# Kernel tuning notes

Hardware: AMD Instinct MI355X
Metric: run time of the kernel (lower is better)

## Reference

```python
import jax, jax.numpy as jnp
import numpy as np

B, SQ, SK, D, N, H = 2, 2048, 2048, 1024, 16, 64
EPS = 1e-5


def setup_inputs() -> dict:
    key = jax.random.key(0)
    ks = jax.random.split(key, 8)
    inv_d = 1.0 / np.sqrt(D)
    inv_h = 1.0 / np.sqrt(H)
    # causal mask: True = masked (filled with -inf), matching torch.where(mask, IGNORE, attn)
    mask = jnp.triu(jnp.ones((SQ, SK), dtype=bool), k=1)
    return {
        "x_q": jax.random.normal(ks[0], (B, SQ, D), dtype=jnp.float32),
        "x_kv": jax.random.normal(ks[1], (B, SK, D), dtype=jnp.float32),
        "mask": mask,
        "W_Q": jax.random.normal(ks[2], (N, D, H), dtype=jnp.float32) * inv_d,
        "W_K": jax.random.normal(ks[3], (N, D, H), dtype=jnp.float32) * inv_d,
        "W_V": jax.random.normal(ks[4], (N, D, H), dtype=jnp.float32) * inv_d,
        "W_O": jax.random.normal(ks[5], (N, H, D), dtype=jnp.float32) * inv_h,
        "b_Q": jnp.zeros((N, H), dtype=jnp.float32),
        "b_K": jnp.zeros((N, H), dtype=jnp.float32),
        "b_V": jnp.zeros((N, H), dtype=jnp.float32),
        "b_O": jnp.zeros((D,), dtype=jnp.float32),
        "ln1_g": jnp.ones((H,), dtype=jnp.float32),
        "ln1_b": jnp.zeros((H,), dtype=jnp.float32),
        "ln2_g": jnp.ones((H,), dtype=jnp.float32),
        "ln2_b": jnp.zeros((H,), dtype=jnp.float32),
    }


def _layernorm(x, g, b):
    # LayerNorm over last dim (d_head), eps=1e-5, biased variance (torch default)
    m = jnp.mean(x, axis=-1, keepdims=True)
    v = jnp.mean(jnp.square(x - m), axis=-1, keepdims=True)
    return (x - m) * jax.lax.rsqrt(v + EPS) * g + b


def reference(x_q, x_kv, mask, W_Q, W_K, W_V, W_O, b_Q, b_K, b_V, b_O,
              ln1_g, ln1_b, ln2_g, ln2_b):
    q = jnp.einsum('bsd,ndh->bsnh', x_q, W_Q) + b_Q    # [B,SQ,N,H]
    k = jnp.einsum('bsd,ndh->bsnh', x_kv, W_K) + b_K   # [B,SK,N,H]
    v = jnp.einsum('bsd,ndh->bsnh', x_kv, W_V) + b_V   # [B,SK,N,H]
    q = _layernorm(q, ln1_g, ln1_b)
    k = _layernorm(k, ln2_g, ln2_b)
    # NOTE: no 1/sqrt(d_head) scaling, faithful to the source module
    attn = jnp.einsum('bqnh,bknh->bnqk', q, k)         # [B,N,SQ,SK]
    attn = jnp.where(mask, -jnp.inf, attn)
    probas = jax.nn.softmax(attn, axis=-1)
    z = jnp.einsum('bnqk,bknh->bqnh', probas, v)       # [B,SQ,N,H]
    out = jnp.einsum('bqnh,nhd->bqd', z, W_O) + b_O    # [B,SQ,D]
    return (out, k, v)
```

## Files before the change

### kernel.cpp

```cpp
#include <hip/hip_runtime.h>
#include <math.h>

namespace {
constexpr int kB  = 2;
constexpr int kS  = 2048;
constexpr int kD  = 1024;
constexpr int kN  = 16;
constexpr int kH  = 64;
constexpr int kBS = kB * kS;
constexpr int kNH = kN * kH;
}

typedef __bf16 bf16x4 __attribute__((ext_vector_type(4)));
typedef __bf16 bf16x8 __attribute__((ext_vector_type(8)));
typedef float  f32x4  __attribute__((ext_vector_type(4)));

__global__ __launch_bounds__(256) void split_x2(
    const float* __restrict__ in0, const float* __restrict__ in1,
    __bf16* __restrict__ oH0, __bf16* __restrict__ oL0,
    __bf16* __restrict__ oH1, __bf16* __restrict__ oL1)
{
  const int bx = blockIdx.x;
  const float* in;
  __bf16 *oH, *oL;
  long long i4;
  if (bx < 4096) { in = in0; oH = oH0; oL = oL0; i4 = (long long)bx * 256 + threadIdx.x; }
  else           { in = in1; oH = oH1; oL = oL1; i4 = (long long)(bx - 4096) * 256 + threadIdx.x; }
  const float4 v = *(const float4*)(in + i4 * 4);
  const float x[4] = {v.x, v.y, v.z, v.w};
  bf16x4 hi, lo;
#pragma unroll
  for (int i = 0; i < 4; ++i) {
    const __bf16 h = (__bf16)x[i];
    hi[i] = h;
    lo[i] = (__bf16)(x[i] - (float)h);
  }
  *(bf16x4*)(oH + i4 * 4) = hi;
  *(bf16x4*)(oL + i4 * 4) = lo;
}

__global__ __launch_bounds__(256) void transpose_split(
    const float* __restrict__ in, long long hsIn, int ldin,
    __bf16* __restrict__ oH, __bf16* __restrict__ oL, long long hsOut)
{
  __shared__ float T[64][65];
  const int t = threadIdx.x;
  const long long inBase = (long long)blockIdx.z * hsIn +
                           (long long)(blockIdx.x * 64) * ldin + blockIdx.y * 64;
  const long long outBase = (long long)blockIdx.z * hsOut +
                            (long long)(blockIdx.y * 64) * 1024 + blockIdx.x * 64;
#pragma unroll
  for (int rr = 0; rr < 4; ++rr) {
    const int i = rr * 16 + (t >> 4);
    const int j = (t & 15) * 4;
    const float4 v = *(const float4*)(in + inBase + (long long)i * ldin + j);
    T[i][j + 0] = v.x; T[i][j + 1] = v.y; T[i][j + 2] = v.z; T[i][j + 3] = v.w;
  }
  __syncthreads();
#pragma unroll
  for (int rr = 0; rr < 4; ++rr) {
    const int hh = rr * 16 + (t >> 4);
    const int kk = (t & 15) * 4;
    bf16x4 hi, lo;
#pragma unroll
    for (int m = 0; m < 4; ++m) {
      const float x = T[kk + m][hh];
      const __bf16 h = (__bf16)x;
      hi[m] = h;
      lo[m] = (__bf16)(x - (float)h);
    }
    *(bf16x4*)(oH + outBase + (long long)hh * 1024 + kk) = hi;
    *(bf16x4*)(oL + outBase + (long long)hh * 1024 + kk) = lo;
  }
}

__global__ __launch_bounds__(256) void transpose_split_qkv(
    const float* __restrict__ WQ, const float* __restrict__ WK,
    const float* __restrict__ WV,
    __bf16* __restrict__ QH, __bf16* __restrict__ QL,
    __bf16* __restrict__ KHo, __bf16* __restrict__ KLo,
    __bf16* __restrict__ VH, __bf16* __restrict__ VL)
{
  __shared__ float T[64][65];
  const int t = threadIdx.x;
  const int which = blockIdx.z >> 4;
  const int z = blockIdx.z & 15;
  const float* __restrict__ in = (which == 0) ? WQ : (which == 1) ? WK : WV;
  __bf16* __restrict__ oH = (which == 0) ? QH : (which == 1) ? KHo : VH;
  __bf16* __restrict__ oL = (which == 0) ? QL : (which == 1) ? KLo : VL;
  const long long inBase = (long long)z * 65536 +
                           (long long)(blockIdx.x * 64) * 64 + blockIdx.y * 64;
  const long long outBase = (long long)z * 65536 +
                            (long long)(blockIdx.y * 64) * 1024 + blockIdx.x * 64;
#pragma unroll
  for (int rr = 0; rr < 4; ++rr) {
    const int i = rr * 16 + (t >> 4);
    const int j = (t & 15) * 4;
    const float4 v = *(const float4*)(in + inBase + (long long)i * 64 + j);
    T[i][j + 0] = v.x; T[i][j + 1] = v.y; T[i][j + 2] = v.z; T[i][j + 3] = v.w;
  }
  __syncthreads();
#pragma unroll
  for (int rr = 0; rr < 4; ++rr) {
    const int hh = rr * 16 + (t >> 4);
    const int kk = (t & 15) * 4;
    bf16x4 hi, lo;
#pragma unroll
    for (int m = 0; m < 4; ++m) {
      const float x = T[kk + m][hh];
      const __bf16 h = (__bf16)x;
      hi[m] = h;
      lo[m] = (__bf16)(x - (float)h);
    }
    *(bf16x4*)(oH + outBase + (long long)hh * 1024 + kk) = hi;
    *(bf16x4*)(oL + outBase + (long long)hh * 1024 + kk) = lo;
  }
}

__global__ __launch_bounds__(256) void qkv_gemm128p(
    const __bf16* __restrict__ xqH, const __bf16* __restrict__ xqL,
    const __bf16* __restrict__ xkH, const __bf16* __restrict__ xkL,
    const __bf16* __restrict__ WQH, const __bf16* __restrict__ WQL,
    const __bf16* __restrict__ WKH, const __bf16* __restrict__ WKL,
    const __bf16* __restrict__ WVH,
    const float* __restrict__ b_Q, const float* __restrict__ b_K,
    const float* __restrict__ b_V,
    const float* __restrict__ ln1g, const float* __restrict__ ln1b,
    const float* __restrict__ ln2g, const float* __restrict__ ln2b,
    float* __restrict__ out_k, float* __restrict__ out_v,
    __bf16* __restrict__ qH, __bf16* __restrict__ qL,
    __bf16* __restrict__ kHp, __bf16* __restrict__ kLp,
    __bf16* __restrict__ vT)
{
  const int mode = blockIdx.z;
  const int row0 = blockIdx.x * 128;
  const int ct   = blockIdx.y;
  const bool split = (mode < 2);

  __shared__ __align__(16) __bf16 SMEM[20480];
  __bf16 (*ASH)[40] = (__bf16(*)[40])(SMEM);
  __bf16 (*ASL)[40] = (__bf16(*)[40])(SMEM + 5120);
  __bf16 (*BSH)[40] = (__bf16(*)[40])(SMEM + 10240);
  __bf16 (*BSL)[40] = (__bf16(*)[40])(SMEM + 15360);

  const int t = threadIdx.x;
  const int lane = t & 63;
  const int w = t >> 6;
  const int l16 = lane & 15;
  const int quad = lane >> 4;
  const int mBase = (w & 1) * 64;
  const int nBase = (w >> 1) * 64;

  const __bf16* __restrict__ aHp = (mode == 0) ? xqH : xkH;
  const __bf16* __restrict__ aLp = (mode == 0) ? xqL : xkL;
  const __bf16* __restrict__ bHp = (mode == 0) ? WQH : (mode == 1) ? WKH : WVH;
  const __bf16* __restrict__ bLp = (mode == 0) ? WQL : WKL;

  f32x4 acc[4][4] = {};

  const int srow = t >> 1;
  const int skh  = (t & 1) * 16;

  bf16x8 r[8];
  auto loadT = [&](int k0, bf16x8 rr[8]) {
    const long long ga = (long long)(row0 + srow) * 1024 + k0 + skh;
    const long long gb = (long long)(ct * 128 + srow) * 1024 + k0 + skh;
    rr[0] = *(const bf16x8*)(aHp + ga);
    rr[1] = *(const bf16x8*)(aHp + ga + 8);
    rr[2] = *(const bf16x8*)(bHp + gb);
    rr[3] = *(const bf16x8*)(bHp + gb + 8);
    if (split) {
      rr[4] = *(const bf16x8*)(aLp + ga);
      rr[5] = *(const bf16x8*)(aLp + ga + 8);
      rr[6] = *(const bf16x8*)(bLp + gb);
      rr[7] = *(const bf16x8*)(bLp + gb + 8);
    }
  };
  loadT(0, r);

  for (int k0 = 0; k0 < 1024; k0 += 32) {
    if (k0) __syncthreads();
    bf16x8 rn[8];
    if (k0 + 32 < 1024) loadT(k0 + 32, rn);
    *(bf16x8*)&ASH[srow][skh]     = r[0];
    *(bf16x8*)&ASH[srow][skh + 8] = r[1];
    *(bf16x8*)&BSH[srow][skh]     = r[2];
    *(bf16x8*)&BSH[srow][skh + 8] = r[3];
    if (split) {
      *(bf16x8*)&ASL[srow][skh]     = r[4];
      *(bf16x8*)&ASL[srow][skh + 8] = r[5];
      *(bf16x8*)&BSL[srow][skh]     = r[6];
      *(bf16x8*)&BSL[srow][skh + 8] = r[7];
    }
    __syncthreads();

    bf16x8 ah[4], bh[4];
#pragma unroll
    for (int mt = 0; mt < 4; ++mt)
      ah[mt] = *(const bf16x8*)&ASH[mBase + mt * 16 + l16][quad * 8];
#pragma unroll
    for (int nt = 0; nt < 4; ++nt)
      bh[nt] = *(const bf16x8*)&BSH[nBase + nt * 16 + l16][quad * 8];
#pragma unroll
    for (int mt = 0; mt < 4; ++mt)
#pragma unroll
      for (int nt = 0; nt < 4; ++nt)
        acc[mt][nt] = __builtin_amdgcn_mfma_f32_16x16x32_bf16(ah[mt], bh[nt], acc[mt][nt], 0, 0, 0);
    if (split) {
      bf16x8 bl[4];
#pragma unroll
      for (int nt = 0; nt < 4; ++nt)
        bl[nt] = *(const bf16x8*)&BSL[nBase + nt * 16 + l16][quad * 8];
#pragma unroll
      for (int mt = 0; mt < 4; ++mt)
#pragma unroll
        for (int nt = 0; nt < 4; ++nt)
          acc[mt][nt] = __builtin_amdgcn_mfma_f32_16x16x32_bf16(ah[mt], bl[nt], acc[mt][nt], 0, 0, 0);
      bf16x8 al[4];
#pragma unroll
      for (int mt = 0; mt < 4; ++mt)
        al[mt] = *(const bf16x8*)&ASL[mBase + mt * 16 + l16][quad * 8];
#pragma unroll
      for (int mt = 0; mt < 4; ++mt)
#pragma unroll
        for (int nt = 0; nt < 4; ++nt)
          acc[mt][nt] = __builtin_amdgcn_mfma_f32_16x16x32_bf16(al[mt], bh[nt], acc[mt][nt], 0, 0, 0);
    }
#pragma unroll
    for (int i = 0; i < 8; ++i) r[i] = rn[i];
  }

  const float* __restrict__ bias = (mode == 0) ? b_Q : (mode == 1) ? b_K : b_V;
  float bi[4];
#pragma unroll
  for (int nt = 0; nt < 4; ++nt) bi[nt] = bias[ct * 128 + nBase + nt * 16 + l16];

  if (mode <= 1) {
    const float* __restrict__ lg = (mode == 0) ? ln1g : ln2g;
    const float* __restrict__ lb = (mode == 0) ? ln1b : ln2b;
    float gg[4], bb[4];
#pragma unroll
    for (int nt = 0; nt < 4; ++nt) {
      gg[nt] = lg[nt * 16 + l16];
      bb[nt] = lb[nt * 16 + l16];
    }
#pragma unroll
    for (int mt = 0; mt < 4; ++mt)
#pragma unroll
      for (int r4 = 0; r4 < 4; ++r4) {
        float y[4];
#pragma unroll
        for (int nt = 0; nt < 4; ++nt) y[nt] = acc[mt][nt][r4] + bi[nt];
        float s = y[0] + y[1] + y[2] + y[3];
#pragma unroll
        for (int o = 8; o >= 1; o >>= 1) s += __shfl_xor(s, o);
        const float m = s * (1.0f / 64.0f);
        float vs = 0.0f;
#pragma unroll
        for (int nt = 0; nt < 4; ++nt) {
          const float d = y[nt] - m;
          vs += d * d;
        }
#pragma unroll
        for (int o = 8; o >= 1; o >>= 1) vs += __shfl_xor(vs, o);
        const float inv = rsqrtf(vs * (1.0f / 64.0f) + 1e-5f);
#pragma unroll
        for (int nt = 0; nt < 4; ++nt)
          acc[mt][nt][r4] = (y[nt] - m) * inv * gg[nt] + bb[nt];
      }
  } else {
#pragma unroll
    for (int mt = 0; mt < 4; ++mt)
#pragma unroll
      for (int nt = 0; nt < 4; ++nt)
#pragma unroll
        for (int r4 = 0; r4 < 4; ++r4) acc[mt][nt][r4] += bi[nt];
  }

#pragma unroll
  for (int mt = 0; mt < 4; ++mt)
#pragma unroll
    for (int r4 = 0; r4 < 4; ++r4) {
      const long long row = row0 + mBase + mt * 16 + quad * 4 + r4;
      const long long cb = row * 1024 + ct * 128 + nBase;
      if (mode == 0) {
#pragma unroll
        for (int nt = 0; nt < 4; ++nt) {
          const float x = acc[mt][nt][r4];
          const __bf16 h = (__bf16)x;
          qH[cb + nt * 16 + l16] = h;
          qL[cb + nt * 16 + l16] = (__bf16)(x - (float)h);
        }
      } else if (mode == 1) {
#pragma unroll
        for (int nt = 0; nt < 4; ++nt) {
          const float x = acc[mt][nt][r4];
          out_k[cb + nt * 16 + l16] = x;
          const __bf16 h = (__bf16)x;
          kHp[cb + nt * 16 + l16] = h;
          kLp[cb + nt * 16 + l16] = (__bf16)(x - (float)h);
        }
      } else {
#pragma unroll
        for (int nt = 0; nt < 4; ++nt)
          out_v[cb + nt * 16 + l16] = acc[mt][nt][r4];
      }
    }

  if (mode == 2) {
    __syncthreads();
    __bf16* TT = SMEM + w * 4608;
#pragma unroll
    for (int mt = 0; mt < 4; ++mt)
#pragma unroll
      for (int nt = 0; nt < 4; ++nt)
#pragma unroll
        for (int r4 = 0; r4 < 4; ++r4)
          TT[(nt * 16 + l16) * 72 + mt * 16 + quad * 4 + r4] = (__bf16)acc[mt][nt][r4];
    __syncthreads();
    const int b = row0 >> 11;
    const int s0 = (row0 + mBase) & 2047;
    const int head = ct * 2 + (w >> 1);
#pragma unroll
    for (int rep = 0; rep < 8; ++rep) {
      const int h = rep * 8 + (lane >> 3);
      const int s8 = (lane & 7) * 8;
      const bf16x8 vv = *(const bf16x8*)&TT[h * 72 + s8];
      *(bf16x8*)(vT + ((long long)((b * 16 + head) * 64 + h)) * 2048 + s0 + s8) = vv;
    }
  }
}

__global__ __launch_bounds__(256) void ogemm64p(
    const __bf16* __restrict__ zH, const __bf16* __restrict__ WOt,
    const float* __restrict__ b_O, float* __restrict__ out)
{
  const int row0 = blockIdx.x * 64;
  const int ct = blockIdx.y;
  __shared__ __align__(16) __bf16 AS2[2][64][40];
  __shared__ __align__(16) __bf16 BS2[2][128][40];
  const int t = threadIdx.x;
  const int lane = t & 63;
  const int w = t >> 6;
  const int l16 = lane & 15;
  const int quad = lane >> 4;
  const int nBase = w * 32;

  f32x4 acc[4][2] = {};
  const int arow = t >> 2, akh = (t & 3) * 8;
  const int brow = t >> 1, bkh = (t & 1) * 16;

  bf16x8 r0, r1, r2;
  auto loadT = [&](int k0) {
    r0 = *(const bf16x8*)(zH + (long long)(row0 + arow) * 1024 + k0 + akh);
    const long long gb = (long long)(ct * 128 + brow) * 1024 + k0 + bkh;
    r1 = *(const bf16x8*)(WOt + gb);
    r2 = *(const bf16x8*)(WOt + gb + 8);
  };
  loadT(0);
  *(bf16x8*)&AS2[0][arow][akh]     = r0;
  *(bf16x8*)&BS2[0][brow][bkh]     = r1;
  *(bf16x8*)&BS2[0][brow][bkh + 8] = r2;
  __syncthreads();

  for (int k0 = 0; k0 < 1024; k0 += 32) {
    const int cb = (k0 >> 5) & 1;
    const bool more = (k0 + 32 < 1024);
    if (more) loadT(k0 + 32);

    bf16x8 ah[4], bh[2];
#pragma unroll
    for (int mt = 0; mt < 4; ++mt)
      ah[mt] = *(const bf16x8*)&AS2[cb][mt * 16 + l16][quad * 8];
#pragma unroll
    for (int nt = 0; nt < 2; ++nt)
      bh[nt] = *(const bf16x8*)&BS2[cb][nBase + nt * 16 + l16][quad * 8];
#pragma unroll
    for (int mt = 0; mt < 4; ++mt)
#pragma unroll
      for (int nt = 0; nt < 2; ++nt)
        acc[mt][nt] = __builtin_amdgcn_mfma_f32_16x16x32_bf16(ah[mt], bh[nt], acc[mt][nt], 0, 0, 0);

    if (more) {
      const int nb = 1 - cb;
      *(bf16x8*)&AS2[nb][arow][akh]     = r0;
      *(bf16x8*)&BS2[nb][brow][bkh]     = r1;
      *(bf16x8*)&BS2[nb][brow][bkh + 8] = r2;
    }
    __syncthreads();
  }

#pragma unroll
  for (int mt = 0; mt < 4; ++mt)
#pragma unroll
    for (int r4 = 0; r4 < 4; ++r4) {
      const long long row = row0 + mt * 16 + quad * 4 + r4;
#pragma unroll
      for (int nt = 0; nt < 2; ++nt) {
        const int col = ct * 128 + nBase + nt * 16 + l16;
        out[row * 1024 + col] = acc[mt][nt][r4] + b_O[col];
      }
    }
}

__global__ __launch_bounds__(256) void attn_mfma3(
    const __bf16* __restrict__ qHg, const __bf16* __restrict__ qLg,
    const __bf16* __restrict__ kHg, const __bf16* __restrict__ kLg,
    const __bf16* __restrict__ vTg,
    __bf16* __restrict__ zH)
{
  const int p = blockIdx.x;
  const int n = blockIdx.y;
  const int b = blockIdx.z;

  __shared__ __align__(16) __bf16 KH[2][64][72];
  __shared__ __align__(16) __bf16 KL[2][64][72];
  __shared__ __align__(16) __bf16 VS[2][64][72];
  __shared__ __align__(16) __bf16 PS[64][72];

  const int t = threadIdx.x;
  const int lane = t & 63;
  const int w = t >> 6;
  const int l16 = lane & 15;
  const int quad = lane >> 4;
  const int skey = t >> 2;
  const int sh16 = (t & 3) * 16;

  for (int half = 0; half < 2; ++half) {
    const int qt = half ? p : (31 - p);
    const int q0 = qt * 64;

    bf16x8 Qh[2], Ql[2];
    {
      const long long qrow = (long long)(b * kS + q0 + w * 16 + l16) * 1024 + n * 64 + quad * 8;
      Qh[0] = *(const bf16x8*)(qHg + qrow);
      Qh[1] = *(const bf16x8*)(qHg + qrow + 32);
      Ql[0] = *(const bf16x8*)(qLg + qrow);
      Ql[1] = *(const bf16x8*)(qLg + qrow + 32);
    }

    f32x4 O[4] = {};
    float mrow[4] = {-3.0e38f, -3.0e38f, -3.0e38f, -3.0e38f};
    float lrow[4] = {};

    bf16x8 rk0, rk1, rl0, rl1, rv0, rv1;
    auto loadKV = [&](int k0) {
      const long long gk = (long long)(b * kS + k0 + skey) * 1024 + n * 64 + sh16;
      rk0 = *(const bf16x8*)(kHg + gk);
      rk1 = *(const bf16x8*)(kHg + gk + 8);
      rl0 = *(const bf16x8*)(kLg + gk);
      rl1 = *(const bf16x8*)(kLg + gk + 8);
      const long long gv = ((long long)(b * kN + n) * 64 + skey) * 2048 + k0 + sh16;
      rv0 = *(const bf16x8*)(vTg + gv);
      rv1 = *(const bf16x8*)(vTg + gv + 8);
    };
    auto storeKV = [&](int buf) {
      *(bf16x8*)&KH[buf][skey][sh16]     = rk0;
      *(bf16x8*)&KH[buf][skey][sh16 + 8] = rk1;
      *(bf16x8*)&KL[buf][skey][sh16]     = rl0;
      *(bf16x8*)&KL[buf][skey][sh16 + 8] = rl1;
      *(bf16x8*)&VS[buf][skey][sh16]     = rv0;
      *(bf16x8*)&VS[buf][skey][sh16 + 8] = rv1;
    };

    loadKV(0);
    storeKV(0);
    __syncthreads();

    for (int kt = 0; kt <= qt; ++kt) {
      const int cb = kt & 1;
      const bool more = (kt < qt);
      if (more) loadKV((kt + 1) * 64);

      f32x4 S[4] = {};
#pragma unroll
      for (int kc = 0; kc < 4; ++kc) {
        const int row = kc * 16 + l16;
        const bf16x8 kh0 = *(const bf16x8*)&KH[cb][row][quad * 8];
        const bf16x8 kh1 = *(const bf16x8*)&KH[cb][row][32 + quad * 8];
        const bf16x8 kl0 = *(const bf16x8*)&KL[cb][row][quad * 8];
        const bf16x8 kl1 = *(const bf16x8*)&KL[cb][row][32 + quad * 8];
        S[kc] = __builtin_amdgcn_mfma_f32_16x16x32_bf16(Qh[0], kh0, S[kc], 0, 0, 0);
        S[kc] = __builtin_amdgcn_mfma_f32_16x16x32_bf16(Qh[1], kh1, S[kc], 0, 0, 0);
        S[kc] = __builtin_amdgcn_mfma_f32_16x16x32_bf16(Qh[0], kl0, S[kc], 0, 0, 0);
        S[kc] = __builtin_amdgcn_mfma_f32_16x16x32_bf16(Qh[1], kl1, S[kc], 0, 0, 0);
        S[kc] = __builtin_amdgcn_mfma_f32_16x16x32_bf16(Ql[0], kh0, S[kc], 0, 0, 0);
        S[kc] = __builtin_amdgcn_mfma_f32_16x16x32_bf16(Ql[1], kh1, S[kc], 0, 0, 0);
      }

      if (kt == qt) {
        const int k0 = kt * 64;
#pragma unroll
        for (int kc = 0; kc < 4; ++kc) {
          const int key = k0 + kc * 16 + l16;
#pragma unroll
          for (int r4 = 0; r4 < 4; ++r4) {
            const int q = q0 + w * 16 + quad * 4 + r4;
            if (key > q) S[kc][r4] = -3.0e38f;
          }
        }
      }

#pragma unroll
      for (int r4 = 0; r4 < 4; ++r4) {
        float mt = fmaxf(fmaxf(S[0][r4], S[1][r4]), fmaxf(S[2][r4], S[3][r4]));
#pragma unroll
        for (int o = 8; o >= 1; o >>= 1) mt = fmaxf(mt, __shfl_xor(mt, o));
        const float mnew = fmaxf(mrow[r4], mt);
        const float alpha = __expf(mrow[r4] - mnew);
        mrow[r4] = mnew;
        float ls = 0.0f;
#pragma unroll
        for (int kc = 0; kc < 4; ++kc) {
          const float pe = __expf(S[kc][r4] - mnew);
          S[kc][r4] = pe;
          ls += pe;
        }
#pragma unroll
        for (int o = 8; o >= 1; o >>= 1) ls += __shfl_xor(ls, o);
        lrow[r4] = lrow[r4] * alpha + ls;
#pragma unroll
        for (int hc = 0; hc < 4; ++hc) O[hc][r4] *= alpha;
      }

#pragma unroll
      for (int kc = 0; kc < 4; ++kc)
#pragma unroll
        for (int r4 = 0; r4 < 4; ++r4)
          PS[w * 16 + quad * 4 + r4][kc * 16 + l16] = (__bf16)S[kc][r4];

      bf16x8 Pa[2];
#pragma unroll
      for (int c = 0; c < 2; ++c)
        Pa[c] = *(const bf16x8*)&PS[w * 16 + l16][c * 32 + quad * 8];
#pragma unroll
      for (int hc = 0; hc < 4; ++hc) {
        const int hrow = hc * 16 + l16;
        const bf16x8 vb0 = *(const bf16x8*)&VS[cb][hrow][quad * 8];
        const bf16x8 vb1 = *(const bf16x8*)&VS[cb][hrow][32 + quad * 8];
        O[hc] = __builtin_amdgcn_mfma_f32_16x16x32_bf16(Pa[0], vb0, O[hc], 0, 0, 0);
        O[hc] = __builtin_amdgcn_mfma_f32_16x16x32_bf16(Pa[1], vb1, O[hc], 0, 0, 0);
      }

      if (more) storeKV(1 - cb);
      __syncthreads();
    }

#pragma unroll
    for (int r4 = 0; r4 < 4; ++r4) {
      const float inv = 1.0f / lrow[r4];
      const long long zrow = (long long)(b * kS + q0 + w * 16 + quad * 4 + r4) * 1024 + n * 64;
#pragma unroll
      for (int hc = 0; hc < 4; ++hc)
        zH[zrow + hc * 16 + l16] = (__bf16)(O[hc][r4] * inv);
    }
  }
}

__global__ __launch_bounds__(256) void sgemm64(
    const float* __restrict__ A, int lda,
    const float* __restrict__ Bbase, long long bStride, int colMul, int ldb,
    float* __restrict__ C, int ldc,
    const float* __restrict__ bias, int K)
{
  const int row0 = blockIdx.x * 64;
  const int ct = blockIdx.y;
  const float* __restrict__ Bp = Bbase + (long long)ct * bStride;
  const int col0B = ct * colMul;
  const int col0C = ct * 64;
  __shared__ float As[16][68];
  __shared__ float Bs[16][68];
  const int t = threadIdx.x;
  const int ty = t >> 4;
  const int tx = t & 15;
  float acc[4][4] = {};
  for (int k0 = 0; k0 < K; k0 += 16) {
    {
      const int r = t >> 2;
      const int kk = (t & 3) * 4;
      const float4 a4 = *(const float4*)(A + (long long)(row0 + r) * lda + k0 + kk);
      As[kk + 0][r] = a4.x; As[kk + 1][r] = a4.y; As[kk + 2][r] = a4.z; As[kk + 3][r] = a4.w;
    }
    {
      const int kk = t >> 4;
      const int c = (t & 15) * 4;
      *(float4*)&Bs[kk][c] = *(const float4*)(Bp + (long long)(k0 + kk) * ldb + col0B + c);
    }
    __syncthreads();
#pragma unroll
    for (int kk = 0; kk < 16; ++kk) {
      const float4 a4 = *(const float4*)&As[kk][ty * 4];
      const float4 b4 = *(const float4*)&Bs[kk][tx * 4];
      const float av[4] = {a4.x, a4.y, a4.z, a4.w};
      const float bv[4] = {b4.x, b4.y, b4.z, b4.w};
#pragma unroll
      for (int i = 0; i < 4; ++i)
#pragma unroll
        for (int j = 0; j < 4; ++j)
          acc[i][j] = fmaf(av[i], bv[j], acc[i][j]);
    }
    __syncthreads();
  }
#pragma unroll
  for (int i = 0; i < 4; ++i) {
    const int r = row0 + ty * 4 + i;
    float4 o;
    o.x = acc[i][0] + bias[col0C + tx * 4 + 0];
    o.y = acc[i][1] + bias[col0C + tx * 4 + 1];
    o.z = acc[i][2] + bias[col0C + tx * 4 + 2];
    o.w = acc[i][3] + bias[col0C + tx * 4 + 3];
    *(float4*)(C + (long long)r * ldc + col0C + tx * 4) = o;
  }
}

__global__ __launch_bounds__(256) void ln64(
    float* __restrict__ X, const float* __restrict__ g,
    const float* __restrict__ bta, int nrows)
{
  const int row = blockIdx.x * 4 + (threadIdx.x >> 6);
  const int lane = threadIdx.x & 63;
  if (row >= nrows) return;
  const float x = X[(long long)row * 64 + lane];
  float s = x;
#pragma unroll
  for (int o = 32; o >= 1; o >>= 1) s += __shfl_xor(s, o);
  const float m = s * (1.0f / 64.0f);
  const float d = x - m;
  float vs = d * d;
#pragma unroll
  for (int o = 32; o >= 1; o >>= 1) vs += __shfl_xor(vs, o);
  const float inv = rsqrtf(vs * (1.0f / 64.0f) + 1e-5f);
  X[(long long)row * 64 + lane] = d * inv * g[lane] + bta[lane];
}

__global__ __launch_bounds__(256) void attn_mfma(
    const float* __restrict__ Q, const float* __restrict__ Kg,
    const float* __restrict__ Vg, float* __restrict__ Z)
{
  const int qt = (gridDim.x - 1) - blockIdx.x;
  const int n = blockIdx.y;
  const int b = blockIdx.z;
  const int q0 = qt * 64;
  __shared__ __bf16 KH[64][72];
  __shared__ __bf16 KL[64][72];
  __shared__ __bf16 VS[64][72];
  const int t = threadIdx.x;
  const int lane = t & 63;
  const int w = t >> 6;
  const int l16 = lane & 15;
  const int quad = lane >> 4;
  bf16x8 Qh[2], Ql[2];
  {
    const long long qrow = ((long long)(b * kS + q0 + w * 16 + l16)) * kNH + n * kH + quad * 8;
#pragma unroll
    for (int c = 0; c < 2; ++c) {
      const float4 a = *(const float4*)(Q + qrow + c * 32);
      const float4 bq = *(const float4*)(Q + qrow + c * 32 + 4);
      const float x[8] = {a.x, a.y, a.z, a.w, bq.x, bq.y, bq.z, bq.w};
#pragma unroll
      for (int i = 0; i < 8; ++i) {
        const __bf16 h = (__bf16)x[i];
        Qh[c][i] = h;
        Ql[c][i] = (__bf16)(x[i] - (float)h);
      }
    }
  }
  f32x4 O[4] = {};
  float mrow[4] = {-3.0e38f, -3.0e38f, -3.0e38f, -3.0e38f};
  float lrow[4] = {};
  for (int kt = 0; kt <= qt; ++kt) {
    const int k0 = kt * 64;
    __syncthreads();
#pragma unroll
    for (int rep = 0; rep < 4; ++rep) {
      {
        const int row = rep * 16 + (t >> 4);
        const int h4 = (t & 15) * 4;
        const float4 k4 = *(const float4*)(Kg + ((long long)(b * kS + k0 + row)) * kNH + n * kH + h4);
        const float x[4] = {k4.x, k4.y, k4.z, k4.w};
        bf16x4 hi, lo;
#pragma unroll
        for (int i = 0; i < 4; ++i) {
          const __bf16 h = (__bf16)x[i];
          hi[i] = h;
          lo[i] = (__bf16)(x[i] - (float)h);
        }
        *(bf16x4*)&KH[row][h4] = hi;
        *(bf16x4*)&KL[row][h4] = lo;
      }
      {
        const int key = rep * 16 + (t & 15);
        const int h4 = (t >> 4) * 4;
        const float4 v4 = *(const float4*)(Vg + ((long long)(b * kS + k0 + key)) * kNH + n * kH + h4);
        VS[h4 + 0][key] = (__bf16)v4.x;
        VS[h4 + 1][key] = (__bf16)v4.y;
        VS[h4 + 2][key] = (__bf16)v4.z;
        VS[h4 + 3][key] = (__bf16)v4.w;
      }
    }
    __syncthreads();
    f32x4 S[4] = {};
#pragma unroll
    for (int kc = 0; kc < 4; ++kc) {
      const int row = kc * 16 + l16;
      const bf16x8 kh0 = *(const bf16x8*)&KH[row][quad * 8];
      const bf16x8 kh1 = *(const bf16x8*)&KH[row][32 + quad * 8];
      const bf16x8 kl0 = *(const bf16x8*)&KL[row][quad * 8];
      const bf16x8 kl1 = *(const bf16x8*)&KL[row][32 + quad * 8];
      S[kc] = __builtin_amdgcn_mfma_f32_16x16x32_bf16(Qh[0], kh0, S[kc], 0, 0, 0);
      S[kc] = __builtin_amdgcn_mfma_f32_16x16x32_bf16(Qh[1], kh1, S[kc], 0, 0, 0);
      S[kc] = __builtin_amdgcn_mfma_f32_16x16x32_bf16(Qh[0], kl0, S[kc], 0, 0, 0);
      S[kc] = __builtin_amdgcn_mfma_f32_16x16x32_bf16(Qh[1], kl1, S[kc], 0, 0, 0);
      S[kc] = __builtin_amdgcn_mfma_f32_16x16x32_bf16(Ql[0], kh0, S[kc], 0, 0, 0);
      S[kc] = __builtin_amdgcn_mfma_f32_16x16x32_bf16(Ql[1], kh1, S[kc], 0, 0, 0);
    }
    if (kt == qt) {
#pragma unroll
      for (int kc = 0; kc < 4; ++kc) {
        const int key = k0 + kc * 16 + l16;
#pragma unroll
        for (int r = 0; r < 4; ++r) {
          const int q = q0 + w * 16 + quad * 4 + r;
          if (key > q) S[kc][r] = -3.0e38f;
        }
      }
    }
#pragma unroll
    for (int r = 0; r < 4; ++r) {
      float mt = fmaxf(fmaxf(S[0][r], S[1][r]), fmaxf(S[2][r], S[3][r]));
#pragma unroll
      for (int o = 8; o >= 1; o >>= 1) mt = fmaxf(mt, __shfl_xor(mt, o));
      const float mnew = fmaxf(mrow[r], mt);
      const float alpha = __expf(mrow[r] - mnew);
      mrow[r] = mnew;
      float ls = 0.0f;
#pragma unroll
      for (int kc = 0; kc < 4; ++kc) {
        const float pe = __expf(S[kc][r] - mnew);
        S[kc][r] = pe;
        ls += pe;
      }
#pragma unroll
      for (int o = 8; o >= 1; o >>= 1) ls += __shfl_xor(ls, o);
      lrow[r] = lrow[r] * alpha + ls;
#pragma unroll
      for (int hc = 0; hc < 4; ++hc) O[hc][r] *= alpha;
    }
    __syncthreads();
    __bf16(*Ps)[72] = KL;
#pragma unroll
    for (int kc = 0; kc < 4; ++kc)
#pragma unroll
      for (int r = 0; r < 4; ++r)
        Ps[w * 16 + quad * 4 + r][kc * 16 + l16] = (__bf16)S[kc][r];
    bf16x8 Pa[2];
#pragma unroll
    for (int c = 0; c < 2; ++c)
      Pa[c] = *(const bf16x8*)&Ps[w * 16 + l16][c * 32 + quad * 8];
#pragma unroll
    for (int hc = 0; hc < 4; ++hc) {
      const int hrow = hc * 16 + l16;
      const bf16x8 vb0 = *(const bf16x8*)&VS[hrow][quad * 8];
      const bf16x8 vb1 = *(const bf16x8*)&VS[hrow][32 + quad * 8];
      O[hc] = __builtin_amdgcn_mfma_f32_16x16x32_bf16(Pa[0], vb0, O[hc], 0, 0, 0);
      O[hc] = __builtin_amdgcn_mfma_f32_16x16x32_bf16(Pa[1], vb1, O[hc], 0, 0, 0);
    }
  }
#pragma unroll
  for (int r = 0; r < 4; ++r) {
    const float inv = 1.0f / lrow[r];
    const long long zrow = ((long long)(b * kS + q0 + w * 16 + quad * 4 + r)) * kNH + n * kH;
#pragma unroll
    for (int hc = 0; hc < 4; ++hc)
      Z[zrow + hc * 16 + l16] = O[hc][r] * inv;
  }
}

extern "C" void kernel_launch(void* const* d_in, const int* in_sizes, int n_in,
                              void* d_out, int out_size, void* d_ws, size_t ws_size,
                              hipStream_t stream)
{
  const float* x_q   = (const float*)d_in[0];
  const float* x_kv  = (const float*)d_in[1];
  const float* W_Q   = (const float*)d_in[3];
  const float* W_K   = (const float*)d_in[4];
  const float* W_V   = (const float*)d_in[5];
  const float* W_O   = (const float*)d_in[6];
  const float* b_Q   = (const float*)d_in[7];
  const float* b_K   = (const float*)d_in[8];
  const float* b_V   = (const float*)d_in[9];
  const float* b_O   = (const float*)d_in[10];
  const float* ln1_g = (const float*)d_in[11];
  const float* ln1_b = (const float*)d_in[12];
  const float* ln2_g = (const float*)d_in[13];
  const float* ln2_b = (const float*)d_in[14];

  float* out_o = (float*)d_out;
  float* out_k = out_o + 4194304;
  float* out_v = out_o + 8388608;

  const dim3 blk(256);

  if (ws_size >= (72ull << 20)) {
    char* W = (char*)d_ws;
    __bf16* xqH = (__bf16*)(W);
    __bf16* xqL = xqH + 4194304;
    __bf16* xkH = (__bf16*)(W + (16ull << 20));
    __bf16* xkL = xkH + 4194304;
    __bf16* wp  = (__bf16*)(W + (32ull << 20));
    __bf16 *WtQH = wp,            *WtQL = wp + 1048576;
    __bf16 *WtKH = wp + 2097152,  *WtKL = wp + 3145728;
    __bf16 *WtVH = wp + 4194304,  *WtVL = wp + 5242880;
    __bf16 *WOtH = wp + 6291456,  *WOtL = wp + 7340032;
    __bf16* kHp = (__bf16*)(W + (48ull << 20));
    __bf16* kLp = kHp + 4194304;
    __bf16* vT  = (__bf16*)(W + (64ull << 20));
    __bf16* zH = xqH;
    __bf16* qH = (__bf16*)out_o;
    __bf16* qL = qH + 4194304;

    hipLaunchKernelGGL(split_x2, dim3(8192), blk, 0, stream,
                       x_q, x_kv, xqH, xqL, xkH, xkL);
    hipLaunchKernelGGL(transpose_split_qkv, dim3(16, 1, 48), blk, 0, stream,
                       W_Q, W_K, W_V, WtQH, WtQL, WtKH, WtKL, WtVH, WtVL);
    hipLaunchKernelGGL(transpose_split, dim3(16, 16, 1), blk, 0, stream,
                       W_O, 0LL, 1024, WOtH, WOtL, 0LL);

    hipLaunchKernelGGL(qkv_gemm128p, dim3(32, 8, 3), blk, 0, stream,
                       xqH, xqL, xkH, xkL,
                       WtQH, WtQL, WtKH, WtKL, WtVH,
                       b_Q, b_K, b_V, ln1_g, ln1_b, ln2_g, ln2_b,
                       out_k, out_v, qH, qL, kHp, kLp, vT);

    hipLaunchKernelGGL(attn_mfma3, dim3(16, 16, 2), blk, 0, stream,
                       qH, qL, kHp, kLp, vT, zH);

    hipLaunchKernelGGL(ogemm64p, dim3(64, 8), blk, 0, stream,
                       zH, WOtH, b_O, out_o);
  } else {
    float* ws_q = out_o;
    float* ws_z = (float*)d_ws;
    const dim3 gproj(kBS / 64, kN);
    hipLaunchKernelGGL(sgemm64, gproj, blk, 0, stream,
                       x_q, kD, W_Q, (long long)kD * kH, 0, kH, ws_q, kNH, b_Q, kD);
    hipLaunchKernelGGL(sgemm64, gproj, blk, 0, stream,
                       x_kv, kD, W_K, (long long)kD * kH, 0, kH, out_k, kNH, b_K, kD);
    hipLaunchKernelGGL(sgemm64, gproj, blk, 0, stream,
                       x_kv, kD, W_V, (long long)kD * kH, 0, kH, out_v, kNH, b_V, kD);
    const int nrows = kBS * kN;
    hipLaunchKernelGGL(ln64, dim3(nrows / 4), blk, 0, stream, ws_q, ln1_g, ln1_b, nrows);
    hipLaunchKernelGGL(ln64, dim3(nrows / 4), blk, 0, stream, out_k, ln2_g, ln2_b, nrows);
    hipLaunchKernelGGL(attn_mfma, dim3(kS / 64, kN, kB), blk, 0, stream,
                       ws_q, out_k, out_v, ws_z);
    hipLaunchKernelGGL(sgemm64, dim3(kBS / 64, kD / 64), blk, 0, stream,
                       ws_z, kNH, W_O, 0LL, 64, kD, out_o, kD, b_O, kD);
  }
}
```

Before: 318.7 us.

## Restructure attention kernel: transposed S, register P, swizzled LDS, one tile per block

The attention kernel now computes S transposed (K as the A operand), so each lane holds a query column. That lets probabilities be packed straight into bf16 MFMA operands in registers, removing the shared-memory P round trip. To match this, the V writer permutes its key ordering. Shared K/V tiles use an XOR-swizzled layout to avoid bank conflicts, and the online-softmax rescale is skipped when no row max changes. The launch goes from paired q-tiles (16 blocks) to one q-tile per block (32 blocks) with occupancy hint 3 and s_setprio around the MFMA sections. This trades the old causal load balancing for more parallelism.

```diff
diff --git a/kernel.cpp b/kernel.cpp
--- a/kernel.cpp
+++ b/kernel.cpp
@@ -14,6 +14,13 @@
 typedef __bf16 bf16x4 __attribute__((ext_vector_type(4)));
 typedef __bf16 bf16x8 __attribute__((ext_vector_type(8)));
 typedef float  f32x4  __attribute__((ext_vector_type(4)));
+typedef unsigned int u32x4 __attribute__((ext_vector_type(4)));
+
+__device__ inline unsigned pkbf(float a, float b) {
+  unsigned short ua = __builtin_bit_cast(unsigned short, (__bf16)a);
+  unsigned short ub = __builtin_bit_cast(unsigned short, (__bf16)b);
+  return (unsigned)ua | ((unsigned)ub << 16);
+}
 
 __global__ __launch_bounds__(256) void split_x2(
     const float* __restrict__ in0, const float* __restrict__ in1,
@@ -326,7 +333,13 @@
       const int h = rep * 8 + (lane >> 3);
       const int s8 = (lane & 7) * 8;
       const bf16x8 vv = *(const bf16x8*)&TT[h * 72 + s8];
-      *(bf16x8*)(vT + ((long long)((b * 16 + head) * 64 + h)) * 2048 + s0 + s8) = vv;
+      const int a  = s8 >> 4;
+      const int c0 = 32 * (a >> 1) + 8 * ((s8 >> 2) & 3) + 4 * (a & 1);
+      __bf16* dst = vT + ((long long)((b * 16 + head) * 64 + h)) * 2048 + s0 + c0;
+      const bf16x4 lo = __builtin_shufflevector(vv, vv, 0, 1, 2, 3);
+      const bf16x4 hi = __builtin_shufflevector(vv, vv, 4, 5, 6, 7);
+      *(bf16x4*)(dst)     = lo;
+      *(bf16x4*)(dst + 8) = hi;
     }
   }
 }
@@ -403,20 +416,18 @@
     }
 }
 
-__global__ __launch_bounds__(256) void attn_mfma3(
+__global__ __launch_bounds__(256, 3) void attn_mfma4(
     const __bf16* __restrict__ qHg, const __bf16* __restrict__ qLg,
     const __bf16* __restrict__ kHg, const __bf16* __restrict__ kLg,
     const __bf16* __restrict__ vTg,
     __bf16* __restrict__ zH)
 {
-  const int p = blockIdx.x;
+  const int qt = 31 - blockIdx.x;
   const int n = blockIdx.y;
   const int b = blockIdx.z;
-
-  __shared__ __align__(16) __bf16 KH[2][64][72];
-  __shared__ __align__(16) __bf16 KL[2][64][72];
-  __shared__ __align__(16) __bf16 VS[2][64][72];
-  __shared__ __align__(16) __bf16 PS[64][72];
+  const int q0 = qt * 64;
+
+  __shared__ __align__(16) char SM[49152];
 
   const int t = threadIdx.x;
   const int lane = t & 63;
@@ -425,135 +436,153 @@
   const int quad = lane >> 4;
   const int skey = t >> 2;
   const int sh16 = (t & 3) * 16;
-
-  for (int half = 0; half < 2; ++half) {
-    const int qt = half ? p : (31 - p);
-    const int q0 = qt * 64;
-
-    bf16x8 Qh[2], Ql[2];
-    {
-      const long long qrow = (long long)(b * kS + q0 + w * 16 + l16) * 1024 + n * 64 + quad * 8;
-      Qh[0] = *(const bf16x8*)(qHg + qrow);
-      Qh[1] = *(const bf16x8*)(qHg + qrow + 32);
-      Ql[0] = *(const bf16x8*)(qLg + qrow);
-      Ql[1] = *(const bf16x8*)(qLg + qrow + 32);
-    }
-
-    f32x4 O[4] = {};
-    float mrow[4] = {-3.0e38f, -3.0e38f, -3.0e38f, -3.0e38f};
-    float lrow[4] = {};
-
-    bf16x8 rk0, rk1, rl0, rl1, rv0, rv1;
-    auto loadKV = [&](int k0) {
-      const long long gk = (long long)(b * kS + k0 + skey) * 1024 + n * 64 + sh16;
-      rk0 = *(const bf16x8*)(kHg + gk);
-      rk1 = *(const bf16x8*)(kHg + gk + 8);
-      rl0 = *(const bf16x8*)(kLg + gk);
-      rl1 = *(const bf16x8*)(kLg + gk + 8);
-      const long long gv = ((long long)(b * kN + n) * 64 + skey) * 2048 + k0 + sh16;
-      rv0 = *(const bf16x8*)(vTg + gv);
-      rv1 = *(const bf16x8*)(vTg + gv + 8);
-    };
-    auto storeKV = [&](int buf) {
-      *(bf16x8*)&KH[buf][skey][sh16]     = rk0;
-      *(bf16x8*)&KH[buf][skey][sh16 + 8] = rk1;
-      *(bf16x8*)&KL[buf][skey][sh16]     = rl0;
-      *(bf16x8*)&KL[buf][skey][sh16 + 8] = rl1;
-      *(bf16x8*)&VS[buf][skey][sh16]     = rv0;
-      *(bf16x8*)&VS[buf][skey][sh16 + 8] = rv1;
-    };
-
-    loadKV(0);
-    storeKV(0);
-    __syncthreads();
-
-    for (int kt = 0; kt <= qt; ++kt) {
-      const int cb = kt & 1;
-      const bool more = (kt < qt);
-      if (more) loadKV((kt + 1) * 64);
-
-      f32x4 S[4] = {};
+  const int su   = sh16 >> 3;
+  const int sx   = (skey & 7) << 4;
+  const int rx   = (l16 & 7) << 4;
+
+  bf16x8 Qh[2], Ql[2];
+  {
+    const long long qrow = (long long)(b * kS + q0 + w * 16 + l16) * 1024 + n * 64 + quad * 8;
+    Qh[0] = *(const bf16x8*)(qHg + qrow);
+    Qh[1] = *(const bf16x8*)(qHg + qrow + 32);
+    Ql[0] = *(const bf16x8*)(qLg + qrow);
+    Ql[1] = *(const bf16x8*)(qLg + qrow + 32);
+  }
+
+  f32x4 O[4] = {};
+  float mrun = -3.0e38f, lrun = 0.0f;
+  const int qg = q0 + w * 16 + l16;
+
+  bf16x8 rk0, rk1, rl0, rl1, rv0, rv1;
+  auto loadKV = [&](int k0) {
+    const long long gk = (long long)(b * kS + k0 + skey) * 1024 + n * 64 + sh16;
+    rk0 = *(const bf16x8*)(kHg + gk);
+    rk1 = *(const bf16x8*)(kHg + gk + 8);
+    rl0 = *(const bf16x8*)(kLg + gk);
+    rl1 = *(const bf16x8*)(kLg + gk + 8);
+    const long long gv = ((long long)(b * kN + n) * 64 + skey) * 2048 + k0 + sh16;
+    rv0 = *(const bf16x8*)(vTg + gv);
+    rv1 = *(const bf16x8*)(vTg + gv + 8);
+  };
+  auto storeKV = [&](int buf) {
+    char* base = SM + buf * 8192 + skey * 128;
+    *(bf16x8*)(base +         (((su    ) << 4) ^ sx)) = rk0;
+    *(bf16x8*)(base +         (((su + 1) << 4) ^ sx)) = rk1;
+    *(bf16x8*)(base + 16384 + (((su    ) << 4) ^ sx)) = rl0;
+    *(bf16x8*)(base + 16384 + (((su + 1) << 4) ^ sx)) = rl1;
+    *(bf16x8*)(base + 32768 + (((su    ) << 4) ^ sx)) = rv0;
+    *(bf16x8*)(base + 32768 + (((su + 1) << 4) ^ sx)) = rv1;
+  };
+
+  loadKV(0);
+  storeKV(0);
+  __syncthreads();
+
+  for (int kt = 0; kt <= qt; ++kt) {
+    const int cb = kt & 1;
+    const bool more = (kt < qt);
+    if (more) loadKV((kt + 1) * 64);
+
+    const char* KHb = SM + cb * 8192;
+    const char* KLb = KHb + 16384;
+    const char* VSb = KHb + 32768;
+
+    f32x4 S[4] = {};
+    __builtin_amdgcn_s_setprio(1);
+#pragma unroll
+    for (int kc = 0; kc < 4; ++kc) {
+      const int ro = (kc * 16 + l16) * 128;
+      const bf16x8 kh0 = *(const bf16x8*)(KHb + ro + (((quad    ) << 4) ^ rx));
+      const bf16x8 kh1 = *(const bf16x8*)(KHb + ro + (((quad + 4) << 4) ^ rx));
+      const bf16x8 kl0 = *(const bf16x8*)(KLb + ro + (((quad    ) << 4) ^ rx));
+      const bf16x8 kl1 = *(const bf16x8*)(KLb + ro + (((quad + 4) << 4) ^ rx));
+      S[kc] = __builtin_amdgcn_mfma_f32_16x16x32_bf16(kh0, Qh[0], S[kc], 0, 0, 0);
+      S[kc] = __builtin_amdgcn_mfma_f32_16x16x32_bf16(kh1, Qh[1], S[kc], 0, 0, 0);
+      S[kc] = __builtin_amdgcn_mfma_f32_16x16x32_bf16(kl0, Qh[0], S[kc], 0, 0, 0);
+      S[kc] = __builtin_amdgcn_mfma_f32_16x16x32_bf16(kl1, Qh[1], S[kc], 0, 0, 0);
+      S[kc] = __builtin_amdgcn_mfma_f32_16x16x32_bf16(kh0, Ql[0], S[kc], 0, 0, 0);
+      S[kc] = __builtin_amdgcn_mfma_f32_16x16x32_bf16(kh1, Ql[1], S[kc], 0, 0, 0);
+    }
+    __builtin_amdgcn_s_setprio(0);
+
+    if (kt == qt) {
 #pragma unroll
       for (int kc = 0; kc < 4; ++kc) {
-        const int row = kc * 16 + l16;
-        const bf16x8 kh0 = *(const bf16x8*)&KH[cb][row][quad * 8];
-        const bf16x8 kh1 = *(const bf16x8*)&KH[cb][row][32 + quad * 8];
-        const bf16x8 kl0 = *(const bf16x8*)&KL[cb][row][quad * 8];
-        const bf16x8 kl1 = *(const bf16x8*)&KL[cb][row][32 + quad * 8];
-        S[kc] = __builtin_amdgcn_mfma_f32_16x16x32_bf16(Qh[0], kh0, S[kc], 0, 0, 0);
-        S[kc] = __builtin_amdgcn_mfma_f32_16x16x32_bf16(Qh[1], kh1, S[kc], 0, 0, 0);
-        S[kc] = __builtin_amdgcn_mfma_f32_16x16x32_bf16(Qh[0], kl0, S[kc], 0, 0, 0);
-        S[kc] = __builtin_amdgcn_mfma_f32_16x16x32_bf16(Qh[1], kl1, S[kc], 0, 0, 0);
-        S[kc] = __builtin_amdgcn_mfma_f32_16x16x32_bf16(Ql[0], kh0, S[kc], 0, 0, 0);
-        S[kc] = __builtin_amdgcn_mfma_f32_16x16x32_bf16(Ql[1], kh1, S[kc], 0, 0, 0);
-      }
-
-      if (kt == qt) {
-        const int k0 = kt * 64;
-#pragma unroll
-        for (int kc = 0; kc < 4; ++kc) {
-          const int key = k0 + kc * 16 + l16;
-#pragma unroll
-          for (int r4 = 0; r4 < 4; ++r4) {
-            const int q = q0 + w * 16 + quad * 4 + r4;
-            if (key > q) S[kc][r4] = -3.0e38f;
-          }
-        }
-      }
-
-#pragma unroll
-      for (int r4 = 0; r4 < 4; ++r4) {
-        float mt = fmaxf(fmaxf(S[0][r4], S[1][r4]), fmaxf(S[2][r4], S[3][r4]));
-#pragma unroll
-        for (int o = 8; o >= 1; o >>= 1) mt = fmaxf(mt, __shfl_xor(mt, o));
-        const float mnew = fmaxf(mrow[r4], mt);
-        const float alpha = __expf(mrow[r4] - mnew);
-        mrow[r4] = mnew;
-        float ls = 0.0f;
-#pragma unroll
-        for (int kc = 0; kc < 4; ++kc) {
-          const float pe = __expf(S[kc][r4] - mnew);
-          S[kc][r4] = pe;
-          ls += pe;
-        }
-#pragma unroll
-        for (int o = 8; o >= 1; o >>= 1) ls += __shfl_xor(ls, o);
-        lrow[r4] = lrow[r4] * alpha + ls;
-#pragma unroll
-        for (int hc = 0; hc < 4; ++hc) O[hc][r4] *= alpha;
-      }
-
-#pragma unroll
-      for (int kc = 0; kc < 4; ++kc)
-#pragma unroll
-        for (int r4 = 0; r4 < 4; ++r4)
-          PS[w * 16 + quad * 4 + r4][kc * 16 + l16] = (__bf16)S[kc][r4];
-
-      bf16x8 Pa[2];
-#pragma unroll
-      for (int c = 0; c < 2; ++c)
-        Pa[c] = *(const bf16x8*)&PS[w * 16 + l16][c * 32 + quad * 8];
-#pragma unroll
-      for (int hc = 0; hc < 4; ++hc) {
-        const int hrow = hc * 16 + l16;
-        const bf16x8 vb0 = *(const bf16x8*)&VS[cb][hrow][quad * 8];
-        const bf16x8 vb1 = *(const bf16x8*)&VS[cb][hrow][32 + quad * 8];
-        O[hc] = __builtin_amdgcn_mfma_f32_16x16x32_bf16(Pa[0], vb0, O[hc], 0, 0, 0);
-        O[hc] = __builtin_amdgcn_mfma_f32_16x16x32_bf16(Pa[1], vb1, O[hc], 0, 0, 0);
-      }
-
-      if (more) storeKV(1 - cb);
-      __syncthreads();
-    }
-
-#pragma unroll
-    for (int r4 = 0; r4 < 4; ++r4) {
-      const float inv = 1.0f / lrow[r4];
-      const long long zrow = (long long)(b * kS + q0 + w * 16 + quad * 4 + r4) * 1024 + n * 64;
+        const int key = q0 + kc * 16 + quad * 4;
+#pragma unroll
+        for (int r = 0; r < 4; ++r)
+          if (key + r > qg) S[kc][r] = -3.0e38f;
+      }
+    }
+
+    float pm = fmaxf(fmaxf(S[0][0], S[0][1]), fmaxf(S[0][2], S[0][3]));
+    pm = fmaxf(pm, fmaxf(fmaxf(S[1][0], S[1][1]), fmaxf(S[1][2], S[1][3])));
+    pm = fmaxf(pm, fmaxf(fmaxf(S[2][0], S[2][1]), fmaxf(S[2][2], S[2][3])));
+    pm = fmaxf(pm, fmaxf(fmaxf(S[3][0], S[3][1]), fmaxf(S[3][2], S[3][3])));
+    pm = fmaxf(pm, __shfl_xor(pm, 16));
+    pm = fmaxf(pm, __shfl_xor(pm, 32));
+    const float mnew = fmaxf(mrun, pm);
+    float ls = 0.0f;
+#pragma unroll
+    for (int kc = 0; kc < 4; ++kc)
+#pragma unroll
+      for (int r = 0; r < 4; ++r) {
+        const float pe = __expf(S[kc][r] - mnew);
+        S[kc][r] = pe;
+        ls += pe;
+      }
+    ls += __shfl_xor(ls, 16);
+    ls += __shfl_xor(ls, 32);
+
+    if (__any(pm > mrun)) {
+      const float alpha = __expf(mrun - mnew);
+      lrun = lrun * alpha + ls;
+      float aB[4];
+#pragma unroll
+      for (int r = 0; r < 4; ++r)
+        aB[r] = __shfl(alpha, (lane & 48) | (quad * 4 + r));
 #pragma unroll
       for (int hc = 0; hc < 4; ++hc)
-        zH[zrow + hc * 16 + l16] = (__bf16)(O[hc][r4] * inv);
-    }
+#pragma unroll
+        for (int r = 0; r < 4; ++r) O[hc][r] *= aB[r];
+    } else {
+      lrun += ls;
+    }
+    mrun = mnew;
+
+    u32x4 pw0, pw1;
+    pw0[0] = pkbf(S[0][0], S[0][1]); pw0[1] = pkbf(S[0][2], S[0][3]);
+    pw0[2] = pkbf(S[1][0], S[1][1]); pw0[3] = pkbf(S[1][2], S[1][3]);
+    pw1[0] = pkbf(S[2][0], S[2][1]); pw1[1] = pkbf(S[2][2], S[2][3]);
+    pw1[2] = pkbf(S[3][0], S[3][1]); pw1[3] = pkbf(S[3][2], S[3][3]);
+    const bf16x8 Pa0 = __builtin_bit_cast(bf16x8, pw0);
+    const bf16x8 Pa1 = __builtin_bit_cast(bf16x8, pw1);
+
+    __builtin_amdgcn_s_setprio(1);
+#pragma unroll
+    for (int hc = 0; hc < 4; ++hc) {
+      const int ro = (hc * 16 + l16) * 128;
+      const bf16x8 vb0 = *(const bf16x8*)(VSb + ro + (((quad    ) << 4) ^ rx));
+      const bf16x8 vb1 = *(const bf16x8*)(VSb + ro + (((quad + 4) << 4) ^ rx));
+      O[hc] = __builtin_amdgcn_mfma_f32_16x16x32_bf16(Pa0, vb0, O[hc], 0, 0, 0);
+      O[hc] = __builtin_amdgcn_mfma_f32_16x16x32_bf16(Pa1, vb1, O[hc], 0, 0, 0);
+    }
+    __builtin_amdgcn_s_setprio(0);
+
+    if (more) storeKV(1 - cb);
+    __syncthreads();
+  }
+
+  float linv[4];
+#pragma unroll
+  for (int r = 0; r < 4; ++r)
+    linv[r] = 1.0f / __shfl(lrun, (lane & 48) | (quad * 4 + r));
+#pragma unroll
+  for (int r = 0; r < 4; ++r) {
+    const long long zrow = (long long)(b * kS + q0 + w * 16 + quad * 4 + r) * 1024 + n * 64;
+#pragma unroll
+    for (int hc = 0; hc < 4; ++hc)
+      zH[zrow + hc * 16 + l16] = (__bf16)(O[hc][r] * linv[r]);
   }
 }
 
@@ -832,7 +861,7 @@
                        b_Q, b_K, b_V, ln1_g, ln1_b, ln2_g, ln2_b,
                        out_k, out_v, qH, qL, kHp, kLp, vT);
 
-    hipLaunchKernelGGL(attn_mfma3, dim3(16, 16, 2), blk, 0, stream,
+    hipLaunchKernelGGL(attn_mfma4, dim3(32, 16, 2), blk, 0, stream,
                        qH, qL, kHp, kLp, vT, zH);
 
     hipLaunchKernelGGL(ogemm64p, dim3(64, 8), blk, 0, stream,
```

Result: slower. 334.9 us (+5.1%).
